# Optimization experiments

Measured on AMD Instinct MI355X. Metric: run time of the kernel, lower is better.

The kernel has to match this reference:

```python
import jax, jax.numpy as jnp
import numpy as np

B, S, D = 8, 2048, 512  # batch, seq_len, dim_val == dim_attn

def setup_inputs() -> dict:
    key = jax.random.key(0)
    kx, kq, kk, kv = jax.random.split(key, 4)
    scale = 1.0 / np.sqrt(D)
    return {
        "x": jax.random.normal(kx, (B, S, D), dtype=jnp.float32),
        "Wq": jax.random.normal(kq, (D, D), dtype=jnp.float32) * scale,  # dim_input -> dim_attn
        "Wk": jax.random.normal(kk, (D, D), dtype=jnp.float32) * scale,
        "Wv": jax.random.normal(kv, (D, D), dtype=jnp.float32) * scale,  # dim_input -> dim_val
    }

def reference(x, Wq, Wk, Wv):
    # bias-free linear projections (nn.Linear stores W as [out,in]; here W is [in,out])
    Q = jnp.einsum("bsd,de->bse", x, Wq)
    K = jnp.einsum("bsd,de->bse", x, Wk)
    V = jnp.einsum("bsd,de->bse", x, Wv)
    # manual scaled dot-product attention: softmax(QK^T / sqrt(d_attn)) V
    scores = jnp.einsum("bqe,bke->bqk", Q, K) / jnp.sqrt(jnp.asarray(Q.shape[-1], Q.dtype))
    a = jax.nn.softmax(scores, axis=-1)
    return jnp.einsum("bqk,bkd->bqd", a, V)
```

## Files before the change

### kernel.cpp

```cpp
#include <hip/hip_runtime.h>


typedef __attribute__((ext_vector_type(8))) short bf16x8;
typedef __attribute__((ext_vector_type(4))) float f32x4;

__device__ __forceinline__ short f2bf(float f) {
  union { float f; unsigned u; } v; v.f = f;
  unsigned r = v.u + 0x7fffu + ((v.u >> 16) & 1u);
  return (short)(r >> 16);
}

__device__ __forceinline__ void async_cp16(const void* g, void* l) {
  __builtin_amdgcn_global_load_lds(
      (const __attribute__((address_space(1))) unsigned int*)g,
      (__attribute__((address_space(3))) unsigned int*)l, 16, 0, 0);
}

__global__ __launch_bounds__(256) void prep_kernel(const float* __restrict__ x,
                                                   const float* __restrict__ Wq,
                                                   const float* __restrict__ Wk,
                                                   const float* __restrict__ Wv,
                                                   short* __restrict__ WT,
                                                   short* __restrict__ xb) {
  if (blockIdx.x < 384) {
    int g = blockIdx.x * 256 + threadIdx.x;
    int w = g >> 15;
    int rem = g & 32767;
    int n = rem & 511;
    int k0 = (rem >> 9) << 3;
    const float* W = (w == 0) ? Wq : ((w == 1) ? Wk : Wv);
    bf16x8 o;
#pragma unroll
    for (int j = 0; j < 8; ++j) o[j] = f2bf(W[(k0 + j) * 512 + n]);
    *(bf16x8*)(WT + w * 262144 + n * 512 + k0) = o;
  } else {
    size_t g = (size_t)(blockIdx.x - 384) * 256 + threadIdx.x;
    size_t off = g * 8;
    f32x4 lo = *(const f32x4*)(x + off);
    f32x4 hi = *(const f32x4*)(x + off + 4);
    bf16x8 o;
    o[0] = f2bf(lo[0]); o[1] = f2bf(lo[1]); o[2] = f2bf(lo[2]); o[3] = f2bf(lo[3]);
    o[4] = f2bf(hi[0]); o[5] = f2bf(hi[1]); o[6] = f2bf(hi[2]); o[7] = f2bf(hi[3]);
    *(bf16x8*)(xb + off) = o;
  }
}

__global__ __launch_bounds__(256, 3) void proj_kernel(const short* __restrict__ xb,
                                                      const short* __restrict__ WT,
                                                      short* __restrict__ QP,
                                                      short* __restrict__ KP,
                                                      short* __restrict__ VP) {
  __shared__ __align__(16) short smem[10240];
  short* Af = smem;
  short* Bf = smem + 4096;
  short* Tb = smem;

  const int tid = threadIdx.x, wv = tid >> 6, ln = tid & 63;
  const int lane_m = ln & 15, lane_q = ln >> 4;
  const int m0 = blockIdx.x * 128, n0 = blockIdx.y * 64;
  const int wm = wv & 1, wn = wv >> 1;

  f32x4 zero4 = {0.f, 0.f, 0.f, 0.f};
  f32x4 acc[3][4][2];
#pragma unroll
  for (int z = 0; z < 3; ++z)
#pragma unroll
    for (int i = 0; i < 4; ++i)
#pragma unroll
      for (int j = 0; j < 2; ++j) acc[z][i][j] = zero4;

#pragma unroll 1
  for (int kk = 0; kk < 16; ++kk) {
    const int k0 = kk * 32;
    __syncthreads();
#pragma unroll
    for (int i = 0; i < 2; ++i) {
      const int mt = wv * 2 + i;
      async_cp16(xb + (size_t)(m0 + mt * 16 + lane_m) * 512 + k0 + lane_q * 8, Af + mt * 512);
    }
#pragma unroll
    for (int z = 0; z < 3; ++z)
      async_cp16(WT + z * 262144 + (size_t)(n0 + wv * 16 + lane_m) * 512 + k0 + lane_q * 8,
                 Bf + z * 2048 + wv * 512);
    __syncthreads();
    bf16x8 a[4];
#pragma unroll
    for (int mi = 0; mi < 4; ++mi) a[mi] = *(bf16x8*)(Af + ((wm * 4 + mi) * 512) + ln * 8);
#pragma unroll
    for (int z = 0; z < 3; ++z) {
      bf16x8 b0 = *(bf16x8*)(Bf + z * 2048 + (wn * 2 + 0) * 512 + ln * 8);
      bf16x8 b1 = *(bf16x8*)(Bf + z * 2048 + (wn * 2 + 1) * 512 + ln * 8);
#pragma unroll
      for (int mi = 0; mi < 4; ++mi) {
        acc[z][mi][0] = __builtin_amdgcn_mfma_f32_16x16x32_bf16(a[mi], b0, acc[z][mi][0], 0, 0, 0);
        acc[z][mi][1] = __builtin_amdgcn_mfma_f32_16x16x32_bf16(a[mi], b1, acc[z][mi][1], 0, 0, 0);
      }
    }
  }

  const int bb = m0 >> 11, tg = (m0 & 2047) >> 6;

#pragma unroll
  for (int z = 0; z < 2; ++z) {
    __syncthreads();
#pragma unroll
    for (int mi = 0; mi < 4; ++mi)
#pragma unroll
      for (int nj = 0; nj < 2; ++nj)
#pragma unroll
        for (int rr = 0; rr < 4; ++rr)
          Tb[(wm * 64 + mi * 16 + lane_q * 4 + rr) * 72 + wn * 32 + nj * 16 + lane_m] =
              f2bf(acc[z][mi][nj][rr]);
    __syncthreads();
    short* Odst = (z == 0) ? QP : KP;
    const int ks0 = n0 >> 5;
#pragma unroll
    for (int p = 0; p < 4; ++p) {
      const int c2 = p * 256 + tid;
      const int ktl = c2 >> 9, wvv = (c2 >> 7) & 3, ksl = (c2 >> 6) & 1;
      const int lq = (c2 >> 4) & 3, lm = c2 & 15;
      const short* src = Tb + (ktl * 64 + wvv * 16 + lm) * 72 + ksl * 32 + lq * 8;
      size_t chunk = (size_t)bb * 131072 + (size_t)(tg + ktl) * 4096 + wvv * 1024 +
                     (ks0 + ksl) * 64 + lq * 16 + lm;
      *(bf16x8*)(Odst + chunk * 8) = *(const bf16x8*)src;
    }
  }
  {
    __syncthreads();
#pragma unroll
    for (int mi = 0; mi < 4; ++mi)
#pragma unroll
      for (int nj = 0; nj < 2; ++nj)
#pragma unroll
        for (int rr = 0; rr < 4; ++rr)
          Tb[(wn * 32 + nj * 16 + lane_m) * 136 + wm * 64 + mi * 16 + lane_q * 4 + rr] =
              f2bf(acc[2][mi][nj][rr]);
    __syncthreads();
    const int wvv2 = n0 >> 7, nt0 = (n0 & 127) >> 4;
#pragma unroll
    for (int p = 0; p < 4; ++p) {
      const int c2 = p * 256 + tid;
      const int ktl = c2 >> 9, ntl = (c2 >> 7) & 3, ks2 = (c2 >> 6) & 1;
      const int lq = (c2 >> 4) & 3, lm = c2 & 15;
      const short* src = Tb + (ntl * 16 + lm) * 136 + ktl * 64 + ks2 * 32 + lq * 8;
      size_t chunk = (size_t)bb * 131072 + (size_t)(tg + ktl) * 4096 + wvv2 * 1024 +
                     (nt0 + ntl) * 128 + ks2 * 64 + lq * 16 + lm;
      *(bf16x8*)(VP + chunk * 8) = *(const bf16x8*)src;
    }
  }
}


#define ISSUE8(R, a0_, a1_, B)                                               \
  asm volatile("global_load_dwordx4 %0, %8, %10\n\t"                         \
               "global_load_dwordx4 %1, %8, %10 offset:1024\n\t"             \
               "global_load_dwordx4 %2, %8, %10 offset:2048\n\t"             \
               "global_load_dwordx4 %3, %8, %10 offset:3072\n\t"             \
               "global_load_dwordx4 %4, %9, %10\n\t"                         \
               "global_load_dwordx4 %5, %9, %10 offset:1024\n\t"             \
               "global_load_dwordx4 %6, %9, %10 offset:2048\n\t"             \
               "global_load_dwordx4 %7, %9, %10 offset:3072\n\t"             \
               : "=&v"(R[0]), "=&v"(R[1]), "=&v"(R[2]), "=&v"(R[3]),         \
                 "=&v"(R[4]), "=&v"(R[5]), "=&v"(R[6]), "=&v"(R[7])          \
               : "v"(a0_), "v"(a1_), "s"(B))

#define WAIT8(R, N)                                                          \
  asm volatile("s_waitcnt vmcnt(" #N ")"                                     \
               : "+v"(R[0]), "+v"(R[1]), "+v"(R[2]), "+v"(R[3]),             \
                 "+v"(R[4]), "+v"(R[5]), "+v"(R[6]), "+v"(R[7]))

#define MFMA(A, B, C) __builtin_amdgcn_mfma_f32_16x16x32_bf16(A, B, C, 0, 0, 0)

#define S_QUARTER(X, ksq)                                                    \
  WAIT8(X, 24);                                                              \
  _Pragma("unroll")                                                          \
  for (int l = 0; l < 4; ++l) {                                              \
    _Pragma("unroll")                                                        \
    for (int mi = 0; mi < 4; ++mi) {                                         \
      bf16x8 a = *(bf16x8*)(qf + ((((ksq)*4 + l) * 4 + mi) * 64 + ln) * 8);  \
      s[mi][0] = MFMA(a, X[l], s[mi][0]);                                    \
      s[mi][1] = MFMA(a, X[4 + l], s[mi][1]);                                \
    }                                                                        \
  }

#define PV_QUARTER(X, vq)                                                    \
  WAIT8(X, 24);                                                              \
  _Pragma("unroll")                                                          \
  for (int ks2 = 0; ks2 < 2; ++ks2) {                                        \
    bf16x8 pa[4];                                                            \
    _Pragma("unroll")                                                        \
    for (int mi = 0; mi < 4; ++mi)                                           \
      pa[mi] = *(bf16x8*)(pfb + ((((vq)*2 + ks2) * 4 + mi) * 64 + effr) * 8);\
    _Pragma("unroll")                                                        \
    for (int ntl = 0; ntl < 4; ++ntl) {                                      \
      _Pragma("unroll")                                                      \
      for (int mi = 0; mi < 4; ++mi)                                         \
        O[mi][ntl] = MFMA(pa[mi], X[ntl * 2 + ks2], O[mi][ntl]);             \
    }                                                                        \
  }

#define ISSUE_KQ(X, kt_, ksq)                                                \
  { const unsigned a0 = kb0 + (unsigned)(((kt_) & 7) * 262144) + (ksq)*4096u;\
    ISSUE8(X, a0, a0 + 16384u, Kp); }

#define ISSUE_VQ(X, kt_, vq)                                                 \
  { const unsigned a0 = vb0 + (unsigned)((kt_) * 262144) + (vq)*65536u;      \
    ISSUE8(X, a0, a0 + 4096u, VTp); }

__global__ __launch_bounds__(512, 2) void flash_kernel(const short* __restrict__ Q,
                                                       const short* __restrict__ K,
                                                       const short* __restrict__ VT,
                                                       float* __restrict__ out) {
  __shared__ __align__(16) short qf[32768];
  __shared__ __align__(16) short pf[32768];
  __shared__ float l_red[8][64];

  const int tid = threadIdx.x, w = tid >> 6, ln = tid & 63;
  const int lane_m = ln & 15, lane_q = ln >> 4;
  const int b = blockIdx.x & 7, qt = blockIdx.x >> 3;
  const int m0 = qt * 64;
  const short* Qp = Q + (size_t)b * 1048576;
  const short* Kp = K + (size_t)b * 1048576;
  const short* VTp = VT + (size_t)b * 1048576;
  const float sc2 = 0.044194173824159216f * 1.4426950408889634f;

#pragma unroll
  for (int r = 0; r < 8; ++r) {
    const int region = w * 8 + r;
    const int mi = region & 3, ks = region >> 2;
    const short* src = Qp + ((size_t)(qt * 4096 + mi * 1024 + ks * 64) + ln) * 8;
    *(bf16x8*)(qf + (region * 64 + ln) * 8) = *(const bf16x8*)src;
  }

  f32x4 zero4 = {0.f, 0.f, 0.f, 0.f};
  f32x4 O[4][4];
#pragma unroll
  for (int mi = 0; mi < 4; ++mi)
#pragma unroll
    for (int ntl = 0; ntl < 4; ++ntl) O[mi][ntl] = zero4;

  float lp[4][4] = {{0.f, 0.f, 0.f, 0.f}, {0.f, 0.f, 0.f, 0.f},
                    {0.f, 0.f, 0.f, 0.f}, {0.f, 0.f, 0.f, 0.f}};

  const unsigned kb0 = (unsigned)((w >> 1) * 65536 + (w & 1) * 32768 + ln * 16);
  const unsigned vb0 = (unsigned)((w >> 1) * 16384 + (w & 1) * 8192 + ln * 16);
  const int jj = lane_m & 7;
  const int effr = ln ^ (ln >> 4);

  __syncthreads();

  bf16x8 bA[8], bB[8], bC[8], bD[8];
  ISSUE_KQ(bA, 0, 0);
  ISSUE_KQ(bB, 0, 1);
  ISSUE_KQ(bC, 0, 2);
  ISSUE_KQ(bD, 0, 3);

#pragma unroll 1
  for (int kt = 0; kt < 8; ++kt) {
    f32x4 s[4][2];
#pragma unroll
    for (int mi = 0; mi < 4; ++mi) { s[mi][0] = zero4; s[mi][1] = zero4; }

    S_QUARTER(bA, 0); ISSUE_VQ(bA, kt, 0);
    S_QUARTER(bB, 1); ISSUE_VQ(bB, kt, 1);
    S_QUARTER(bC, 2); ISSUE_VQ(bC, kt, 2);
    S_QUARTER(bD, 3); ISSUE_VQ(bD, kt, 3);

    short* pfb = pf + (kt & 1) * 16384;
#pragma unroll
    for (int mi = 0; mi < 4; ++mi)
#pragma unroll
      for (int kj = 0; kj < 2; ++kj) {
        const int quad = (kj << 1) | (lane_m >> 3);
#pragma unroll
        for (int rr = 0; rr < 4; ++rr) {
          const int m = lane_q * 4 + rr;
          const int eff = (m ^ quad) + quad * 16;
          float p = exp2f(s[mi][kj][rr] * sc2 - 12.0f);
          lp[mi][rr] += p;
          pfb[((w * 4 + mi) * 64 + eff) * 8 + jj] = f2bf(p);
        }
      }
    asm volatile("s_waitcnt lgkmcnt(0)" ::: "memory");
    __builtin_amdgcn_s_barrier();
    asm volatile("" ::: "memory");

    PV_QUARTER(bA, 0); ISSUE_KQ(bA, kt + 1, 0);
    PV_QUARTER(bB, 1); ISSUE_KQ(bB, kt + 1, 1);
    PV_QUARTER(bC, 2); ISSUE_KQ(bC, kt + 1, 2);
    PV_QUARTER(bD, 3); ISSUE_KQ(bD, kt + 1, 3);
  }
  WAIT8(bA, 0);
  WAIT8(bB, 0);
  WAIT8(bC, 0);
  WAIT8(bD, 0);

#pragma unroll
  for (int mi = 0; mi < 4; ++mi)
#pragma unroll
    for (int rr = 0; rr < 4; ++rr) {
      float v = lp[mi][rr];
      v += __shfl_xor(v, 1);
      v += __shfl_xor(v, 2);
      v += __shfl_xor(v, 4);
      v += __shfl_xor(v, 8);
      lp[mi][rr] = v;
    }
  if (lane_m == 0) {
#pragma unroll
    for (int mi = 0; mi < 4; ++mi)
#pragma unroll
      for (int rr = 0; rr < 4; ++rr)
        l_red[w][mi * 16 + lane_q * 4 + rr] = lp[mi][rr];
  }
  __syncthreads();

  float linv[4][4];
#pragma unroll
  for (int mi = 0; mi < 4; ++mi)
#pragma unroll
    for (int rr = 0; rr < 4; ++rr) {
      const int row = mi * 16 + lane_q * 4 + rr;
      float l = 0.f;
#pragma unroll
      for (int ww = 0; ww < 8; ++ww) l += l_red[ww][row];
      linv[mi][rr] = 1.f / l;
    }
#pragma unroll
  for (int mi = 0; mi < 4; ++mi)
#pragma unroll
    for (int ntl = 0; ntl < 4; ++ntl)
#pragma unroll
      for (int rr = 0; rr < 4; ++rr) {
        size_t row = (size_t)b * 2048 + m0 + mi * 16 + lane_q * 4 + rr;
        out[row * 512 + w * 64 + ntl * 16 + lane_m] = O[mi][ntl][rr] * linv[mi][rr];
      }
}

extern "C" void kernel_launch(void* const* d_in, const int* in_sizes, int n_in,
                              void* d_out, int out_size, void* d_ws, size_t ws_size,
                              hipStream_t stream) {
  const float* x  = (const float*)d_in[0];
  const float* Wq = (const float*)d_in[1];
  const float* Wk = (const float*)d_in[2];
  const float* Wv = (const float*)d_in[3];
  float* out = (float*)d_out;
  char* ws = (char*)d_ws;
  short* WT = (short*)ws;
  short* QP = (short*)(ws + 1572864);
  short* KP = (short*)(ws + 1572864 + 16777216);
  short* VP = (short*)(ws + 1572864 + 2 * 16777216);
  short* xb = (short*)(ws + 1572864 + 3 * 16777216);

  prep_kernel<<<dim3(384 + 4096), dim3(256), 0, stream>>>(x, Wq, Wk, Wv, WT, xb);
  proj_kernel<<<dim3(128, 8), dim3(256), 0, stream>>>(xb, WT, QP, KP, VP);
  flash_kernel<<<dim3(256), dim3(512), 0, stream>>>(QP, KP, VP, out);
}
```

Before: 243.7 us.

## Switch attention kernel to 32x32x16 MFMA with triple-buffered K/V register pipeline

Replaces the 16x16x32 MFMA tiling in the attention kernel with 32x32x16 MFMA, and changes the Q/K/V packed layouts written by the projection kernel to match the new fragment shapes. The K/V register prefetch drops from four buffers to three, rotated across a 3-way unrolled loop with interleaved issue points. The softmax probabilities are stored as 4-wide vectors, and the row-sum reduction is simplified. The aim is fewer MFMA instructions per FLOP, fewer LDS fragment reads, and lower register pressure, at the cost of a more complex rotation schedule and new swizzle and padding choices that may cause bank conflicts.

```diff
diff --git a/kernel.cpp b/kernel.cpp
--- a/kernel.cpp
+++ b/kernel.cpp
@@ -2,7 +2,9 @@
 
 
 typedef __attribute__((ext_vector_type(8))) short bf16x8;
+typedef __attribute__((ext_vector_type(4))) short short4v;
 typedef __attribute__((ext_vector_type(4))) float f32x4;
+typedef __attribute__((ext_vector_type(16))) float f32x16;
 
 __device__ __forceinline__ short f2bf(float f) {
   union { float f; unsigned u; } v; v.f = f;
@@ -98,7 +100,7 @@
     }
   }
 
-  const int bb = m0 >> 11, tg = (m0 & 2047) >> 6;
+  const int bb = m0 >> 11;
 
 #pragma unroll
   for (int z = 0; z < 2; ++z) {
@@ -109,20 +111,19 @@
       for (int nj = 0; nj < 2; ++nj)
 #pragma unroll
         for (int rr = 0; rr < 4; ++rr)
-          Tb[(wm * 64 + mi * 16 + lane_q * 4 + rr) * 72 + wn * 32 + nj * 16 + lane_m] =
+          Tb[(wm * 64 + mi * 16 + lane_q * 4 + rr) * 68 + wn * 32 + nj * 16 + lane_m] =
               f2bf(acc[z][mi][nj][rr]);
     __syncthreads();
     short* Odst = (z == 0) ? QP : KP;
-    const int ks0 = n0 >> 5;
+    const int g0 = (m0 & 2047) >> 5, kst0 = n0 >> 4;
 #pragma unroll
     for (int p = 0; p < 4; ++p) {
       const int c2 = p * 256 + tid;
-      const int ktl = c2 >> 9, wvv = (c2 >> 7) & 3, ksl = (c2 >> 6) & 1;
-      const int lq = (c2 >> 4) & 3, lm = c2 & 15;
-      const short* src = Tb + (ktl * 64 + wvv * 16 + lm) * 72 + ksl * 32 + lq * 8;
-      size_t chunk = (size_t)bb * 131072 + (size_t)(tg + ktl) * 4096 + wvv * 1024 +
-                     (ks0 + ksl) * 64 + lq * 16 + lm;
-      *(bf16x8*)(Odst + chunk * 8) = *(const bf16x8*)src;
+      const int frag = c2 >> 6, ln2 = c2 & 63;
+      const int gl = frag >> 2, kl = frag & 3;
+      const short* src = Tb + (gl * 32 + (ln2 & 31)) * 68 + kl * 16 + ((ln2 >> 5) << 3);
+      size_t dst = (size_t)bb * 1048576 + (size_t)((g0 + gl) * 32 + kst0 + kl) * 512 + ln2 * 8;
+      *(bf16x8*)(Odst + dst) = *(const bf16x8*)src;
     }
   }
   {
@@ -133,19 +134,18 @@
       for (int nj = 0; nj < 2; ++nj)
 #pragma unroll
         for (int rr = 0; rr < 4; ++rr)
-          Tb[(wn * 32 + nj * 16 + lane_m) * 136 + wm * 64 + mi * 16 + lane_q * 4 + rr] =
+          Tb[(wn * 32 + nj * 16 + lane_m) * 132 + wm * 64 + mi * 16 + lane_q * 4 + rr] =
               f2bf(acc[2][mi][nj][rr]);
     __syncthreads();
-    const int wvv2 = n0 >> 7, nt0 = (n0 & 127) >> 4;
+    const int ng0 = n0 >> 5, kv0 = (m0 & 2047) >> 4;
 #pragma unroll
     for (int p = 0; p < 4; ++p) {
       const int c2 = p * 256 + tid;
-      const int ktl = c2 >> 9, ntl = (c2 >> 7) & 3, ks2 = (c2 >> 6) & 1;
-      const int lq = (c2 >> 4) & 3, lm = c2 & 15;
-      const short* src = Tb + (ntl * 16 + lm) * 136 + ktl * 64 + ks2 * 32 + lq * 8;
-      size_t chunk = (size_t)bb * 131072 + (size_t)(tg + ktl) * 4096 + wvv2 * 1024 +
-                     (nt0 + ntl) * 128 + ks2 * 64 + lq * 16 + lm;
-      *(bf16x8*)(VP + chunk * 8) = *(const bf16x8*)src;
+      const int frag = c2 >> 6, ln2 = c2 & 63;
+      const int ngl = frag >> 3, kvl = frag & 7;
+      const short* src = Tb + (ngl * 32 + (ln2 & 31)) * 132 + kvl * 16 + ((ln2 >> 5) << 3);
+      size_t dst = (size_t)bb * 1048576 + (size_t)((ng0 + ngl) * 128 + kv0 + kvl) * 512 + ln2 * 8;
+      *(bf16x8*)(VP + dst) = *(const bf16x8*)src;
     }
   }
 }
@@ -169,43 +169,79 @@
                : "+v"(R[0]), "+v"(R[1]), "+v"(R[2]), "+v"(R[3]),             \
                  "+v"(R[4]), "+v"(R[5]), "+v"(R[6]), "+v"(R[7]))
 
-#define MFMA(A, B, C) __builtin_amdgcn_mfma_f32_16x16x32_bf16(A, B, C, 0, 0, 0)
-
-#define S_QUARTER(X, ksq)                                                    \
-  WAIT8(X, 24);                                                              \
+#define MFMA32(A, B, C) __builtin_amdgcn_mfma_f32_32x32x16_bf16(A, B, C, 0, 0, 0)
+
+#define ISSUE_KQ(X, kt_, qq)                                                 \
+  { const unsigned a0 = kb0 + (unsigned)(((kt_) & 7) * 262144) + (qq) * 8192u; \
+    ISSUE8(X, a0, a0 + 4096u, Kp); }
+
+#define ISSUE_VQ(X, kt_, vq)                                                 \
+  { const unsigned a0 = vb0 + (unsigned)((kt_) * 16384) + (vq) * 4096u;      \
+    ISSUE8(X, a0, a0 + 131072u, VTp); }
+
+#define S_QUARTER(X, qq)                                                     \
+  WAIT8(X, 16);                                                              \
   _Pragma("unroll")                                                          \
-  for (int l = 0; l < 4; ++l) {                                              \
+  for (int c = 0; c < 8; ++c) {                                              \
+    const int kst = (qq) * 8 + c;                                            \
+    bf16x8 bq0 = *(bf16x8*)(qf + kst * 512 + ln * 8);                        \
+    bf16x8 bq1 = *(bf16x8*)(qf + (32 + kst) * 512 + ln * 8);                 \
+    s0 = MFMA32(X[c], bq0, s0);                                              \
+    s1 = MFMA32(X[c], bq1, s1);                                              \
+  }
+
+#define PV_QUARTER(X, vq)                                                    \
+  WAIT8(X, 16);                                                              \
+  _Pragma("unroll")                                                          \
+  for (int c = 0; c < 4; ++c) {                                              \
+    const int kbg = (vq) * 4 + c;                                            \
+    bf16x8 pa0 = *(bf16x8*)(pfb + kbg * 512 + ln * 8);                       \
+    bf16x8 pa1 = *(bf16x8*)(pfb + (16 + kbg) * 512 + ln * 8);                \
+    O00 = MFMA32(pa0, X[c], O00);                                            \
+    O01 = MFMA32(pa0, X[4 + c], O01);                                        \
+    O10 = MFMA32(pa1, X[c], O10);                                            \
+    O11 = MFMA32(pa1, X[4 + c], O11);                                        \
+  }
+
+#define SOFTMAX(kt_)                                                         \
+  pfb = pf + ((kt_) & 1) * 16384;                                            \
+  {                                                                          \
+    float p0[16], p1[16];                                                    \
     _Pragma("unroll")                                                        \
-    for (int mi = 0; mi < 4; ++mi) {                                         \
-      bf16x8 a = *(bf16x8*)(qf + ((((ksq)*4 + l) * 4 + mi) * 64 + ln) * 8);  \
-      s[mi][0] = MFMA(a, X[l], s[mi][0]);                                    \
-      s[mi][1] = MFMA(a, X[4 + l], s[mi][1]);                                \
+    for (int r = 0; r < 16; ++r) {                                           \
+      p0[r] = exp2f(s0[r] * sc2 - 12.0f);                                    \
+      p1[r] = exp2f(s1[r] * sc2 - 12.0f);                                    \
+      lp0 += p0[r];                                                          \
+      lp1 += p1[r];                                                          \
     }                                                                        \
-  }
-
-#define PV_QUARTER(X, vq)                                                    \
-  WAIT8(X, 24);                                                              \
-  _Pragma("unroll")                                                          \
-  for (int ks2 = 0; ks2 < 2; ++ks2) {                                        \
-    bf16x8 pa[4];                                                            \
     _Pragma("unroll")                                                        \
-    for (int mi = 0; mi < 4; ++mi)                                           \
-      pa[mi] = *(bf16x8*)(pfb + ((((vq)*2 + ks2) * 4 + mi) * 64 + effr) * 8);\
-    _Pragma("unroll")                                                        \
-    for (int ntl = 0; ntl < 4; ++ntl) {                                      \
+    for (int kbl = 0; kbl < 2; ++kbl)                                        \
       _Pragma("unroll")                                                      \
-      for (int mi = 0; mi < 4; ++mi)                                         \
-        O[mi][ntl] = MFMA(pa[mi], X[ntl * 2 + ks2], O[mi][ntl]);             \
-    }                                                                        \
-  }
-
-#define ISSUE_KQ(X, kt_, ksq)                                                \
-  { const unsigned a0 = kb0 + (unsigned)(((kt_) & 7) * 262144) + (ksq)*4096u;\
-    ISSUE8(X, a0, a0 + 16384u, Kp); }
-
-#define ISSUE_VQ(X, kt_, vq)                                                 \
-  { const unsigned a0 = vb0 + (unsigned)((kt_) * 262144) + (vq)*65536u;      \
-    ISSUE8(X, a0, a0 + 4096u, VTp); }
+      for (int hk = 0; hk < 2; ++hk) {                                       \
+        const int br = kbl * 8 + hk * 4;                                     \
+        short4v v0c = {f2bf(p0[br]), f2bf(p0[br + 1]), f2bf(p0[br + 2]), f2bf(p0[br + 3])}; \
+        short4v v1c = {f2bf(p1[br]), f2bf(p1[br + 1]), f2bf(p1[br + 2]), f2bf(p1[br + 3])}; \
+        *(short4v*)(pfb + (w * 2 + kbl) * 512 + (q32 + 32 * hk) * 8 + 4 * hq) = v0c;        \
+        *(short4v*)(pfb + (16 + w * 2 + kbl) * 512 + (q32 + 32 * hk) * 8 + 4 * hq) = v1c;   \
+      }                                                                      \
+  }                                                                          \
+  asm volatile("s_waitcnt lgkmcnt(0)" ::: "memory");                         \
+  __builtin_amdgcn_s_barrier();                                              \
+  asm volatile("" ::: "memory");
+
+#define ITER(X, Y, Z, kt_)                                                   \
+  {                                                                          \
+    f32x16 s0 = zz, s1 = zz;                                                 \
+    S_QUARTER(X, 0); ISSUE_KQ(X, kt_, 3);                                    \
+    S_QUARTER(Y, 1); ISSUE_VQ(Y, kt_, 0);                                    \
+    S_QUARTER(Z, 2); ISSUE_VQ(Z, kt_, 1);                                    \
+    S_QUARTER(X, 3); ISSUE_VQ(X, kt_, 2);                                    \
+    SOFTMAX(kt_);                                                            \
+    PV_QUARTER(Y, 0); ISSUE_VQ(Y, kt_, 3);                                   \
+    PV_QUARTER(Z, 1); ISSUE_KQ(Z, (kt_) + 1, 0);                             \
+    PV_QUARTER(X, 2); ISSUE_KQ(X, (kt_) + 1, 1);                             \
+    PV_QUARTER(Y, 3); ISSUE_KQ(Y, (kt_) + 1, 2);                             \
+  }
 
 __global__ __launch_bounds__(512, 2) void flash_kernel(const short* __restrict__ Q,
                                                        const short* __restrict__ K,
@@ -214,9 +250,10 @@
   __shared__ __align__(16) short qf[32768];
   __shared__ __align__(16) short pf[32768];
   __shared__ float l_red[8][64];
+  __shared__ float lsum[64];
 
   const int tid = threadIdx.x, w = tid >> 6, ln = tid & 63;
-  const int lane_m = ln & 15, lane_q = ln >> 4;
+  const int q32 = ln & 31, hq = ln >> 5;
   const int b = blockIdx.x & 7, qt = blockIdx.x >> 3;
   const int m0 = qt * 64;
   const short* Qp = Q + (size_t)b * 1048576;
@@ -226,115 +263,70 @@
 
 #pragma unroll
   for (int r = 0; r < 8; ++r) {
-    const int region = w * 8 + r;
-    const int mi = region & 3, ks = region >> 2;
-    const short* src = Qp + ((size_t)(qt * 4096 + mi * 1024 + ks * 64) + ln) * 8;
-    *(bf16x8*)(qf + (region * 64 + ln) * 8) = *(const bf16x8*)src;
-  }
-
-  f32x4 zero4 = {0.f, 0.f, 0.f, 0.f};
-  f32x4 O[4][4];
-#pragma unroll
-  for (int mi = 0; mi < 4; ++mi)
-#pragma unroll
-    for (int ntl = 0; ntl < 4; ++ntl) O[mi][ntl] = zero4;
-
-  float lp[4][4] = {{0.f, 0.f, 0.f, 0.f}, {0.f, 0.f, 0.f, 0.f},
-                    {0.f, 0.f, 0.f, 0.f}, {0.f, 0.f, 0.f, 0.f}};
-
-  const unsigned kb0 = (unsigned)((w >> 1) * 65536 + (w & 1) * 32768 + ln * 16);
-  const unsigned vb0 = (unsigned)((w >> 1) * 16384 + (w & 1) * 8192 + ln * 16);
-  const int jj = lane_m & 7;
-  const int effr = ln ^ (ln >> 4);
+    const int reg = w * 8 + r;
+    *(bf16x8*)(qf + reg * 512 + ln * 8) =
+        *(const bf16x8*)(Qp + (size_t)(qt * 64 + reg) * 512 + ln * 8);
+  }
+
+  f32x16 zz = {};
+  f32x16 O00 = zz, O01 = zz, O10 = zz, O11 = zz;
+  float lp0 = 0.f, lp1 = 0.f;
+  short* pfb = pf;
+
+  const unsigned kb0 = (unsigned)(w * 32768 + ln * 16);
+  const unsigned vb0 = (unsigned)(w * 262144 + ln * 16);
 
   __syncthreads();
 
-  bf16x8 bA[8], bB[8], bC[8], bD[8];
+  bf16x8 bA[8], bB[8], bC[8];
   ISSUE_KQ(bA, 0, 0);
   ISSUE_KQ(bB, 0, 1);
   ISSUE_KQ(bC, 0, 2);
-  ISSUE_KQ(bD, 0, 3);
 
 #pragma unroll 1
-  for (int kt = 0; kt < 8; ++kt) {
-    f32x4 s[4][2];
-#pragma unroll
-    for (int mi = 0; mi < 4; ++mi) { s[mi][0] = zero4; s[mi][1] = zero4; }
-
-    S_QUARTER(bA, 0); ISSUE_VQ(bA, kt, 0);
-    S_QUARTER(bB, 1); ISSUE_VQ(bB, kt, 1);
-    S_QUARTER(bC, 2); ISSUE_VQ(bC, kt, 2);
-    S_QUARTER(bD, 3); ISSUE_VQ(bD, kt, 3);
-
-    short* pfb = pf + (kt & 1) * 16384;
-#pragma unroll
-    for (int mi = 0; mi < 4; ++mi)
-#pragma unroll
-      for (int kj = 0; kj < 2; ++kj) {
-        const int quad = (kj << 1) | (lane_m >> 3);
-#pragma unroll
-        for (int rr = 0; rr < 4; ++rr) {
-          const int m = lane_q * 4 + rr;
-          const int eff = (m ^ quad) + quad * 16;
-          float p = exp2f(s[mi][kj][rr] * sc2 - 12.0f);
-          lp[mi][rr] += p;
-          pfb[((w * 4 + mi) * 64 + eff) * 8 + jj] = f2bf(p);
-        }
-      }
-    asm volatile("s_waitcnt lgkmcnt(0)" ::: "memory");
-    __builtin_amdgcn_s_barrier();
-    asm volatile("" ::: "memory");
-
-    PV_QUARTER(bA, 0); ISSUE_KQ(bA, kt + 1, 0);
-    PV_QUARTER(bB, 1); ISSUE_KQ(bB, kt + 1, 1);
-    PV_QUARTER(bC, 2); ISSUE_KQ(bC, kt + 1, 2);
-    PV_QUARTER(bD, 3); ISSUE_KQ(bD, kt + 1, 3);
-  }
-  WAIT8(bA, 0);
+  for (int tt = 0; tt < 2; ++tt) {
+    const int kt = tt * 3;
+    ITER(bA, bB, bC, kt);
+    ITER(bC, bA, bB, kt + 1);
+    ITER(bB, bC, bA, kt + 2);
+  }
+  ITER(bA, bB, bC, 6);
+  ITER(bC, bA, bB, 7);
+
   WAIT8(bB, 0);
   WAIT8(bC, 0);
-  WAIT8(bD, 0);
-
-#pragma unroll
-  for (int mi = 0; mi < 4; ++mi)
-#pragma unroll
-    for (int rr = 0; rr < 4; ++rr) {
-      float v = lp[mi][rr];
-      v += __shfl_xor(v, 1);
-      v += __shfl_xor(v, 2);
-      v += __shfl_xor(v, 4);
-      v += __shfl_xor(v, 8);
-      lp[mi][rr] = v;
-    }
-  if (lane_m == 0) {
-#pragma unroll
-    for (int mi = 0; mi < 4; ++mi)
-#pragma unroll
-      for (int rr = 0; rr < 4; ++rr)
-        l_red[w][mi * 16 + lane_q * 4 + rr] = lp[mi][rr];
+  WAIT8(bA, 0);
+
+  lp0 += __shfl_xor(lp0, 32);
+  lp1 += __shfl_xor(lp1, 32);
+  if (ln < 32) {
+    l_red[w][q32] = lp0;
+    l_red[w][32 + q32] = lp1;
   }
   __syncthreads();
-
-  float linv[4][4];
-#pragma unroll
-  for (int mi = 0; mi < 4; ++mi)
-#pragma unroll
-    for (int rr = 0; rr < 4; ++rr) {
-      const int row = mi * 16 + lane_q * 4 + rr;
-      float l = 0.f;
-#pragma unroll
-      for (int ww = 0; ww < 8; ++ww) l += l_red[ww][row];
-      linv[mi][rr] = 1.f / l;
-    }
-#pragma unroll
-  for (int mi = 0; mi < 4; ++mi)
-#pragma unroll
-    for (int ntl = 0; ntl < 4; ++ntl)
-#pragma unroll
-      for (int rr = 0; rr < 4; ++rr) {
-        size_t row = (size_t)b * 2048 + m0 + mi * 16 + lane_q * 4 + rr;
-        out[row * 512 + w * 64 + ntl * 16 + lane_m] = O[mi][ntl][rr] * linv[mi][rr];
+  if (tid < 64) {
+    float s = 0.f;
+#pragma unroll
+    for (int ww = 0; ww < 8; ++ww) s += l_red[ww][tid];
+    lsum[tid] = s;
+  }
+  __syncthreads();
+
+#pragma unroll
+  for (int qb = 0; qb < 2; ++qb)
+#pragma unroll
+    for (int r = 0; r < 16; ++r) {
+      const int row = qb * 32 + (r & 3) + 8 * (r >> 2) + 4 * hq;
+      const float li = 1.f / lsum[row];
+      const size_t ro = ((size_t)b * 2048 + m0 + row) * 512 + w * 64 + q32;
+      if (qb == 0) {
+        out[ro] = O00[r] * li;
+        out[ro + 32] = O01[r] * li;
+      } else {
+        out[ro] = O10[r] * li;
+        out[ro + 32] = O11[r] * li;
       }
+    }
 }
 
 extern "C" void kernel_launch(void* const* d_in, const int* in_sizes, int n_in,
```

Measured after the change: 216.6 us. 11.2% less time.
